# Performance work log

Hardware: AMD Instinct MI355X
Metric: run time of the kernel (lower is better)

Reference implementation:

```python
import jax, jax.numpy as jnp
import numpy as np

B, D, K, L, H = 16384, 1024, 512, 128, 64  # batch, input_dim, num_components, latent_dim, phi hidden
EPS = 1e-9


def setup_inputs() -> dict:
    key = jax.random.key(0)
    k0, k1, k2, k3 = jax.random.split(key, 4)
    # small scales keep squared distances O(1-10) so exp(-d2) is non-degenerate
    x = jax.random.normal(k0, (B, D), jnp.float32) * 0.03
    z_samples = jax.random.normal(k1, (K, L), jnp.float32)
    W1 = jax.random.normal(k2, (L, H), jnp.float32) * (1.0 / np.sqrt(L)).astype(np.float32)
    b1 = jnp.zeros((H,), jnp.float32)
    W2 = jax.random.normal(k3, (H, D), jnp.float32) * 0.01
    b2 = jnp.zeros((D,), jnp.float32)
    return {"x": x, "z_samples": z_samples, "W1": W1, "b1": b1, "W2": W2, "b2": b2}


def reference(x, z_samples, W1, b1, W2, b2):
    # PhiNet: Linear -> ReLU -> Linear, applied to all components at once
    phi = jnp.maximum(z_samples @ W1 + b1, 0.0) @ W2 + b2          # (K, D)
    # ||x - phi_k||^2 for all (k, b) via GEMM expansion (fuses the per-component loop)
    sq = (jnp.sum(phi * phi, axis=-1)[:, None]
          + jnp.sum(x * x, axis=-1)[None, :]
          - 2.0 * (phi @ x.T))                                      # (K, B)
    lik = jnp.exp(-sq)                                              # (K, B)
    # weights = 1/K; sum_k w * lik = mean over K
    mixture_ll = jnp.log(jnp.mean(lik, axis=0) + EPS)               # (B,)
    return mixture_ll.mean()
```

## Files before the change

### kernel.cpp

```cpp
#include <hip/hip_runtime.h>
#include <hip/hip_bf16.h>
#include <stdint.h>

#define N_B   16384
#define D_DIM 1024
#define K_K   512
#define L_DIM 128
#define H_DIM 64
#define SX    1032

typedef __attribute__((ext_vector_type(8))) short short8;
typedef __attribute__((ext_vector_type(4))) float f32x4;

__device__ __forceinline__ unsigned short f2bf(float f) {
    union { float f; unsigned int u; } c; c.f = f;
    unsigned int u = c.u;
    unsigned int r = (u + 0x7FFFu + ((u >> 16) & 1u)) >> 16;
    return (unsigned short)r;
}

__device__ __forceinline__ unsigned int pk2(float a, float b) {
    __hip_bfloat162 t = __float22bfloat162_rn(make_float2(a, b));
    union { __hip_bfloat162 h; unsigned int u; } c; c.h = t;
    return c.u;
}

__global__ __launch_bounds__(256) void prep_kernel(
    const float* __restrict__ z, const float* __restrict__ W1,
    const float* __restrict__ b1, const float* __restrict__ W2,
    const float* __restrict__ b2, unsigned short* __restrict__ W2bf,
    unsigned short* __restrict__ h_bf, float* __restrict__ phi2) {
    __shared__ float zsh[8][L_DIM];
    __shared__ float hsh[8][H_DIM];
    __shared__ float redp[4][8];
    const int tid = threadIdx.x;
    const int k0 = blockIdx.x * 8;

    {
        int i = blockIdx.x * 256 + tid;
        float4 v = ((const float4*)W2)[i];
        uint2 o = make_uint2(pk2(v.x, v.y), pk2(v.z, v.w));
        *(uint2*)(W2bf + i * 4) = o;
    }
#pragma unroll
    for (int c = 0; c < 4; ++c) {
        int idx = c * 256 + tid;
        zsh[idx >> 7][idx & 127] = z[k0 * L_DIM + idx];
    }
    __syncthreads();
    {
        const int j = tid & 63, kk = tid >> 6;
        float bb = b1[j];
        float s0 = bb, s1 = bb;
        for (int l = 0; l < L_DIM; ++l) {
            float w = W1[l * H_DIM + j];
            s0 += zsh[kk][l] * w;
            s1 += zsh[kk + 4][l] * w;
        }
        float h0 = fmaxf(s0, 0.0f), h1 = fmaxf(s1, 0.0f);
        hsh[kk][j] = h0; hsh[kk + 4][j] = h1;
        h_bf[(k0 + kk) * H_DIM + j]     = f2bf(h0);
        h_bf[(k0 + kk + 4) * H_DIM + j] = f2bf(h1);
    }
    __syncthreads();
    float ss[8] = {0.f, 0.f, 0.f, 0.f, 0.f, 0.f, 0.f, 0.f};
#pragma unroll
    for (int c = 0; c < 4; ++c) {
        int d = c * 256 + tid;
        float bb = b2[d];
        float a[8];
#pragma unroll
        for (int kk = 0; kk < 8; ++kk) a[kk] = bb;
        for (int j = 0; j < H_DIM; ++j) {
            float w = W2[j * D_DIM + d];
#pragma unroll
            for (int kk = 0; kk < 8; ++kk) a[kk] += hsh[kk][j] * w;
        }
#pragma unroll
        for (int kk = 0; kk < 8; ++kk) ss[kk] += a[kk] * a[kk];
    }
    const int lane = tid & 63, wv = tid >> 6;
#pragma unroll
    for (int kk = 0; kk < 8; ++kk) {
        float v = ss[kk];
#pragma unroll
        for (int o = 1; o < 64; o <<= 1) v += __shfl_xor(v, o, 64);
        if (lane == 0) redp[wv][kk] = v;
    }
    __syncthreads();
    if (tid < 8) phi2[k0 + tid] = redp[0][tid] + redp[1][tid] + redp[2][tid] + redp[3][tid];
}

__global__ __launch_bounds__(256) void main_kernel(
    const float* __restrict__ x, const unsigned short* __restrict__ W2bf,
    const unsigned short* __restrict__ h_bf, const float* __restrict__ phi2,
    const float* __restrict__ b2, float* __restrict__ out) {
    __shared__ __align__(16) unsigned short x_bf[32 * SX];
    __shared__ __align__(16) unsigned short u_tile[32 * 72];
    __shared__ float phi2s[K_K];
    __shared__ float x2s[32], xb2s[32];
    __shared__ float red[4][32];

    const int tid = threadIdx.x;
    const int wv  = tid >> 6;
    const int l   = tid & 63;
    const int lm  = l & 15;
    const int q   = l >> 4;
    const int n0  = blockIdx.x * 32;

    float4 b2r[4];
#pragma unroll
    for (int sub = 0; sub < 4; ++sub)
        b2r[sub] = ((const float4*)b2)[sub * 64 + l];

    float x2a[8], xba[8];
#pragma unroll
    for (int it = 0; it < 8; ++it) {
        const int r = it * 4 + wv;
        const float* xrow = x + (size_t)(n0 + r) * D_DIM;
        float s2 = 0.f, sb = 0.f;
#pragma unroll
        for (int sub = 0; sub < 4; ++sub) {
            float4 v = *(const float4*)(xrow + sub * 256 + l * 4);
            s2 += v.x*v.x + v.y*v.y + v.z*v.z + v.w*v.w;
            sb += v.x*b2r[sub].x + v.y*b2r[sub].y + v.z*b2r[sub].z + v.w*b2r[sub].w;
            uint2 o = make_uint2(pk2(v.x, v.y), pk2(v.z, v.w));
            *(uint2*)&x_bf[r * SX + sub * 256 + l * 4] = o;
        }
        x2a[it] = s2; xba[it] = sb;
    }
    phi2s[tid]       = phi2[tid];
    phi2s[256 + tid] = phi2[256 + tid];
#pragma unroll
    for (int it = 0; it < 8; ++it) {
        float a = x2a[it], b = xba[it];
#pragma unroll
        for (int o = 1; o < 64; o <<= 1) { a += __shfl_xor(a, o, 64); b += __shfl_xor(b, o, 64); }
        if (l == 0) { x2s[it * 4 + wv] = a; xb2s[it * 4 + wv] = b; }
    }
    __syncthreads();

    f32x4 c1[2] = {};
    const unsigned short* w2row = W2bf + (size_t)(wv * 16 + lm) * D_DIM;
#pragma unroll
    for (int ks = 0; ks < 32; ++ks) {
        const int k0 = ks * 32 + q * 8;
        short8 bw = *(const short8*)(w2row + k0);
        short8 a0 = *(const short8*)&x_bf[lm * SX + k0];
        short8 a1 = *(const short8*)&x_bf[(16 + lm) * SX + k0];
        c1[0] = __builtin_amdgcn_mfma_f32_16x16x32_bf16(a0, bw, c1[0], 0, 0, 0);
        c1[1] = __builtin_amdgcn_mfma_f32_16x16x32_bf16(a1, bw, c1[1], 0, 0, 0);
    }
#pragma unroll
    for (int i = 0; i < 2; ++i)
#pragma unroll
        for (int r = 0; r < 4; ++r)
            u_tile[(i * 16 + q * 4 + r) * 72 + wv * 16 + lm] = f2bf(c1[i][r]);
    __syncthreads();

    f32x4 acc[8][2] = {};
#pragma unroll
    for (int ks = 0; ks < 2; ++ks) {
        const int ko = ks * 32 + q * 8;
        short8 bfr[2];
#pragma unroll
        for (int j = 0; j < 2; ++j)
            bfr[j] = *(const short8*)&u_tile[(j * 16 + lm) * 72 + ko];
#pragma unroll
        for (int i = 0; i < 8; ++i) {
            short8 a = *(const short8*)(h_bf + (size_t)(wv * 128 + i * 16 + lm) * H_DIM + ko);
#pragma unroll
            for (int j = 0; j < 2; ++j)
                acc[i][j] = __builtin_amdgcn_mfma_f32_16x16x32_bf16(a, bfr[j], acc[i][j], 0, 0, 0);
        }
    }
    float xn0 = x2s[lm]      - 2.f * xb2s[lm];
    float xn1 = x2s[16 + lm] - 2.f * xb2s[16 + lm];
    float cs0 = 0.f, cs1 = 0.f;
#pragma unroll
    for (int i = 0; i < 8; ++i) {
#pragma unroll
        for (int r = 0; r < 4; ++r) {
            float p2 = phi2s[wv * 128 + i * 16 + q * 4 + r];
            cs0 += __expf(-(p2 + xn0 - 2.f * acc[i][0][r]));
            cs1 += __expf(-(p2 + xn1 - 2.f * acc[i][1][r]));
        }
    }
    cs0 += __shfl_xor(cs0, 16, 64); cs0 += __shfl_xor(cs0, 32, 64);
    cs1 += __shfl_xor(cs1, 16, 64); cs1 += __shfl_xor(cs1, 32, 64);
    if (l < 16) { red[wv][l] = cs0; red[wv][16 + l] = cs1; }
    __syncthreads();
    if (tid < 32) {
        float row_lik = red[0][tid] + red[1][tid] + red[2][tid] + red[3][tid];
        float lg = __logf(row_lik * (1.0f / (float)K_K) + 1e-9f);
        lg += __shfl_xor(lg, 1, 64);
        lg += __shfl_xor(lg, 2, 64);
        lg += __shfl_xor(lg, 4, 64);
        lg += __shfl_xor(lg, 8, 64);
        lg += __shfl_xor(lg, 16, 64);
        if (tid == 0) atomicAdd(out, lg * (1.0f / (float)N_B));
    }
}

extern "C" void kernel_launch(void* const* d_in, const int* in_sizes, int n_in,
                              void* d_out, int out_size, void* d_ws, size_t ws_size,
                              hipStream_t stream) {
    const float* x  = (const float*)d_in[0];
    const float* z  = (const float*)d_in[1];
    const float* W1 = (const float*)d_in[2];
    const float* b1 = (const float*)d_in[3];
    const float* W2 = (const float*)d_in[4];
    const float* b2 = (const float*)d_in[5];

    char* ws = (char*)d_ws;
    unsigned short* W2bf = (unsigned short*)(ws);
    unsigned short* h_bf = (unsigned short*)(ws + 131072);
    float*          phi2 = (float*)(ws + 196608);

    hipMemsetAsync(d_out, 0, sizeof(float), stream);
    prep_kernel<<<64, 256, 0, stream>>>(z, W1, b1, W2, b2, W2bf, h_bf, phi2);
    main_kernel<<<N_B / 32, 256, 0, stream>>>(x, W2bf, h_bf, phi2, b2, (float*)d_out);
}
```

Measured before the change: 146.2 us.

## Halve rows per block to 16 and batch x loads for more occupancy

Cuts the batch rows handled per main_kernel block from 32 to 16, which halves LDS use and accumulator registers and doubles the grid. Adds launch_bounds with min 4 blocks per CU, and loads the x row fragments in two batches of eight float4 to raise memory-level parallelism. The cost is that each block now reloads W2bf and h_bf for half as many rows, doubling that traffic from cache, and issues twice as many atomics.

```diff
diff --git a/kernel.cpp b/kernel.cpp
--- a/kernel.cpp
+++ b/kernel.cpp
@@ -91,113 +91,108 @@
     if (tid < 8) phi2[k0 + tid] = redp[0][tid] + redp[1][tid] + redp[2][tid] + redp[3][tid];
 }
 
-__global__ __launch_bounds__(256) void main_kernel(
+__global__ __launch_bounds__(256, 4) void main_kernel(
     const float* __restrict__ x, const unsigned short* __restrict__ W2bf,
     const unsigned short* __restrict__ h_bf, const float* __restrict__ phi2,
     const float* __restrict__ b2, float* __restrict__ out) {
-    __shared__ __align__(16) unsigned short x_bf[32 * SX];
-    __shared__ __align__(16) unsigned short u_tile[32 * 72];
+    __shared__ __align__(16) unsigned short x_bf[16 * SX];
+    __shared__ __align__(16) unsigned short u_tile[16 * 72];
     __shared__ float phi2s[K_K];
-    __shared__ float x2s[32], xb2s[32];
-    __shared__ float red[4][32];
+    __shared__ float x2s[16], xb2s[16];
+    __shared__ float red[4][16];
 
     const int tid = threadIdx.x;
     const int wv  = tid >> 6;
     const int l   = tid & 63;
     const int lm  = l & 15;
     const int q   = l >> 4;
-    const int n0  = blockIdx.x * 32;
+    const int n0  = blockIdx.x * 16;
 
     float4 b2r[4];
 #pragma unroll
     for (int sub = 0; sub < 4; ++sub)
         b2r[sub] = ((const float4*)b2)[sub * 64 + l];
 
-    float x2a[8], xba[8];
-#pragma unroll
-    for (int it = 0; it < 8; ++it) {
-        const int r = it * 4 + wv;
-        const float* xrow = x + (size_t)(n0 + r) * D_DIM;
-        float s2 = 0.f, sb = 0.f;
-#pragma unroll
-        for (int sub = 0; sub < 4; ++sub) {
-            float4 v = *(const float4*)(xrow + sub * 256 + l * 4);
-            s2 += v.x*v.x + v.y*v.y + v.z*v.z + v.w*v.w;
-            sb += v.x*b2r[sub].x + v.y*b2r[sub].y + v.z*b2r[sub].z + v.w*b2r[sub].w;
-            uint2 o = make_uint2(pk2(v.x, v.y), pk2(v.z, v.w));
-            *(uint2*)&x_bf[r * SX + sub * 256 + l * 4] = o;
-        }
-        x2a[it] = s2; xba[it] = sb;
-    }
     phi2s[tid]       = phi2[tid];
     phi2s[256 + tid] = phi2[256 + tid];
-#pragma unroll
-    for (int it = 0; it < 8; ++it) {
-        float a = x2a[it], b = xba[it];
+
+    float x2a[4] = {0.f, 0.f, 0.f, 0.f}, xba[4] = {0.f, 0.f, 0.f, 0.f};
+#pragma unroll
+    for (int half = 0; half < 2; ++half) {
+        float4 xv[8];
+#pragma unroll
+        for (int s = 0; s < 4; ++s)
+#pragma unroll
+            for (int p = 0; p < 2; ++p) {
+                const int sub = half * 2 + p;
+                xv[s * 2 + p] = *(const float4*)(x + (size_t)(n0 + s * 4 + wv) * D_DIM + sub * 256 + l * 4);
+            }
+#pragma unroll
+        for (int s = 0; s < 4; ++s)
+#pragma unroll
+            for (int p = 0; p < 2; ++p) {
+                const int sub = half * 2 + p;
+                float4 v = xv[s * 2 + p];
+                x2a[s] += v.x*v.x + v.y*v.y + v.z*v.z + v.w*v.w;
+                xba[s] += v.x*b2r[sub].x + v.y*b2r[sub].y + v.z*b2r[sub].z + v.w*b2r[sub].w;
+                uint2 o = make_uint2(pk2(v.x, v.y), pk2(v.z, v.w));
+                *(uint2*)&x_bf[(s * 4 + wv) * SX + sub * 256 + l * 4] = o;
+            }
+    }
+#pragma unroll
+    for (int s = 0; s < 4; ++s) {
+        float a = x2a[s], b = xba[s];
 #pragma unroll
         for (int o = 1; o < 64; o <<= 1) { a += __shfl_xor(a, o, 64); b += __shfl_xor(b, o, 64); }
-        if (l == 0) { x2s[it * 4 + wv] = a; xb2s[it * 4 + wv] = b; }
-    }
-    __syncthreads();
-
-    f32x4 c1[2] = {};
+        if (l == 0) { x2s[s * 4 + wv] = a; xb2s[s * 4 + wv] = b; }
+    }
+    __syncthreads();
+
+    f32x4 c1 = {};
     const unsigned short* w2row = W2bf + (size_t)(wv * 16 + lm) * D_DIM;
 #pragma unroll
     for (int ks = 0; ks < 32; ++ks) {
         const int k0 = ks * 32 + q * 8;
         short8 bw = *(const short8*)(w2row + k0);
         short8 a0 = *(const short8*)&x_bf[lm * SX + k0];
-        short8 a1 = *(const short8*)&x_bf[(16 + lm) * SX + k0];
-        c1[0] = __builtin_amdgcn_mfma_f32_16x16x32_bf16(a0, bw, c1[0], 0, 0, 0);
-        c1[1] = __builtin_amdgcn_mfma_f32_16x16x32_bf16(a1, bw, c1[1], 0, 0, 0);
-    }
-#pragma unroll
-    for (int i = 0; i < 2; ++i)
-#pragma unroll
-        for (int r = 0; r < 4; ++r)
-            u_tile[(i * 16 + q * 4 + r) * 72 + wv * 16 + lm] = f2bf(c1[i][r]);
-    __syncthreads();
-
-    f32x4 acc[8][2] = {};
+        c1 = __builtin_amdgcn_mfma_f32_16x16x32_bf16(a0, bw, c1, 0, 0, 0);
+    }
+#pragma unroll
+    for (int r = 0; r < 4; ++r)
+        u_tile[(q * 4 + r) * 72 + wv * 16 + lm] = f2bf(c1[r]);
+    __syncthreads();
+
+    f32x4 acc[8] = {};
 #pragma unroll
     for (int ks = 0; ks < 2; ++ks) {
         const int ko = ks * 32 + q * 8;
-        short8 bfr[2];
-#pragma unroll
-        for (int j = 0; j < 2; ++j)
-            bfr[j] = *(const short8*)&u_tile[(j * 16 + lm) * 72 + ko];
+        short8 bfr = *(const short8*)&u_tile[lm * 72 + ko];
 #pragma unroll
         for (int i = 0; i < 8; ++i) {
             short8 a = *(const short8*)(h_bf + (size_t)(wv * 128 + i * 16 + lm) * H_DIM + ko);
-#pragma unroll
-            for (int j = 0; j < 2; ++j)
-                acc[i][j] = __builtin_amdgcn_mfma_f32_16x16x32_bf16(a, bfr[j], acc[i][j], 0, 0, 0);
-        }
-    }
-    float xn0 = x2s[lm]      - 2.f * xb2s[lm];
-    float xn1 = x2s[16 + lm] - 2.f * xb2s[16 + lm];
-    float cs0 = 0.f, cs1 = 0.f;
+            acc[i] = __builtin_amdgcn_mfma_f32_16x16x32_bf16(a, bfr, acc[i], 0, 0, 0);
+        }
+    }
+    float xn = x2s[lm] - 2.f * xb2s[lm];
+    float cs = 0.f;
 #pragma unroll
     for (int i = 0; i < 8; ++i) {
 #pragma unroll
         for (int r = 0; r < 4; ++r) {
             float p2 = phi2s[wv * 128 + i * 16 + q * 4 + r];
-            cs0 += __expf(-(p2 + xn0 - 2.f * acc[i][0][r]));
-            cs1 += __expf(-(p2 + xn1 - 2.f * acc[i][1][r]));
-        }
-    }
-    cs0 += __shfl_xor(cs0, 16, 64); cs0 += __shfl_xor(cs0, 32, 64);
-    cs1 += __shfl_xor(cs1, 16, 64); cs1 += __shfl_xor(cs1, 32, 64);
-    if (l < 16) { red[wv][l] = cs0; red[wv][16 + l] = cs1; }
-    __syncthreads();
-    if (tid < 32) {
+            cs += __expf(-(p2 + xn - 2.f * acc[i][r]));
+        }
+    }
+    cs += __shfl_xor(cs, 16, 64); cs += __shfl_xor(cs, 32, 64);
+    if (l < 16) red[wv][l] = cs;
+    __syncthreads();
+    if (tid < 16) {
         float row_lik = red[0][tid] + red[1][tid] + red[2][tid] + red[3][tid];
         float lg = __logf(row_lik * (1.0f / (float)K_K) + 1e-9f);
         lg += __shfl_xor(lg, 1, 64);
         lg += __shfl_xor(lg, 2, 64);
         lg += __shfl_xor(lg, 4, 64);
         lg += __shfl_xor(lg, 8, 64);
-        lg += __shfl_xor(lg, 16, 64);
         if (tid == 0) atomicAdd(out, lg * (1.0f / (float)N_B));
     }
 }
@@ -219,5 +214,5 @@
 
     hipMemsetAsync(d_out, 0, sizeof(float), stream);
     prep_kernel<<<64, 256, 0, stream>>>(z, W1, b1, W2, b2, W2bf, h_bf, phi2);
-    main_kernel<<<N_B / 32, 256, 0, stream>>>(x, W2bf, h_bf, phi2, b2, (float*)d_out);
-}
+    main_kernel<<<N_B / 16, 256, 0, stream>>>(x, W2bf, h_bf, phi2, b2, (float*)d_out);
+}
```

After: 155.1 us. +6.1%, slower.
